# Kernel tuning notes

Hardware: AMD Instinct MI355X
Metric: run time of the kernel (lower is better)

## Reference

```python
import jax, jax.numpy as jnp
import numpy as np

T, I, H, O = 8192, 512, 1024, 2


def setup_inputs() -> dict:
    key = jax.random.key(0)
    ks = jax.random.split(key, 7)
    s_ih = 1.0 / np.sqrt(H)
    return {
        "input_seq": jax.random.normal(ks[0], (T, I), dtype=jnp.float32),
        "W_ih": jax.random.normal(ks[1], (4 * H, I), dtype=jnp.float32) * s_ih,
        "W_hh": jax.random.normal(ks[2], (4 * H, H), dtype=jnp.float32) * s_ih,
        "b_ih": jax.random.normal(ks[3], (4 * H,), dtype=jnp.float32) * s_ih,
        "b_hh": jax.random.normal(ks[4], (4 * H,), dtype=jnp.float32) * s_ih,
        "W_lin": jax.random.normal(ks[5], (O, H), dtype=jnp.float32) * s_ih,
        "b_lin": jax.random.normal(ks[6], (O,), dtype=jnp.float32) * s_ih,
    }


def reference(input_seq, W_ih, W_hh, b_ih, b_hh, W_lin, b_lin):
    h0 = jnp.zeros((H,), dtype=input_seq.dtype)
    c0 = jnp.zeros((H,), dtype=input_seq.dtype)
    # Precompute input projections for all timesteps: (T, 4H)
    x_gates = input_seq @ W_ih.T + b_ih + b_hh

    def step(carry, xg):
        h, c = carry
        gates = xg + h @ W_hh.T  # (4H,) in PyTorch order i, f, g, o
        i_g, f_g, g_g, o_g = jnp.split(gates, 4)
        i_g = jax.nn.sigmoid(i_g)
        f_g = jax.nn.sigmoid(f_g)
        g_g = jnp.tanh(g_g)
        o_g = jax.nn.sigmoid(o_g)
        c_new = f_g * c + i_g * g_g
        h_new = o_g * jnp.tanh(c_new)
        return (h_new, c_new), h_new

    _, hs = jax.lax.scan(step, (h0, c0), x_gates)  # hs: (T, H)
    logits = hs @ W_lin.T + b_lin  # (T, O)
    return jax.nn.softmax(logits, axis=-1)
```

## Files before the change

### kernel.cpp

```cpp
#include <hip/hip_runtime.h>
#include <stdint.h>

#define T_STEPS 8192
#define IN_DIM  512
#define HID     1024
#define G4      4096
#define NBLK    64
#define NW      16

typedef unsigned long long u64;

__global__ __launch_bounds__(256) void gemm_xgates(
    const float* __restrict__ A,
    const float* __restrict__ W,
    const float* __restrict__ bih,
    const float* __restrict__ bhh,
    float* __restrict__ xg)
{
    __shared__ float At[8][128];
    __shared__ float Bt[8][128];
    const int tid = threadIdx.x;
    const int r0 = blockIdx.x * 128;
    const int t0 = blockIdx.y * 128;
    const int tx = tid & 15, ty = tid >> 4;
    const int lrow = tid >> 1;
    const int kq   = (tid & 1) * 4;

    float acc[8][8];
#pragma unroll
    for (int i = 0; i < 8; ++i)
#pragma unroll
        for (int j = 0; j < 8; ++j) acc[i][j] = 0.f;

    for (int k0 = 0; k0 < IN_DIM; k0 += 8) {
        float4 av = *(const float4*)&A[(size_t)(t0 + lrow) * IN_DIM + k0 + kq];
        float4 bv = *(const float4*)&W[(size_t)(r0 + lrow) * IN_DIM + k0 + kq];
        __syncthreads();
        At[kq + 0][lrow] = av.x; At[kq + 1][lrow] = av.y;
        At[kq + 2][lrow] = av.z; At[kq + 3][lrow] = av.w;
        Bt[kq + 0][lrow] = bv.x; Bt[kq + 1][lrow] = bv.y;
        Bt[kq + 2][lrow] = bv.z; Bt[kq + 3][lrow] = bv.w;
        __syncthreads();
#pragma unroll
        for (int k = 0; k < 8; ++k) {
            float4 a0 = *(const float4*)&At[k][ty * 8];
            float4 a1 = *(const float4*)&At[k][ty * 8 + 4];
            float4 b0 = *(const float4*)&Bt[k][tx * 8];
            float4 b1 = *(const float4*)&Bt[k][tx * 8 + 4];
            float aa[8] = {a0.x, a0.y, a0.z, a0.w, a1.x, a1.y, a1.z, a1.w};
            float bb[8] = {b0.x, b0.y, b0.z, b0.w, b1.x, b1.y, b1.z, b1.w};
#pragma unroll
            for (int i = 0; i < 8; ++i)
#pragma unroll
                for (int j = 0; j < 8; ++j) acc[i][j] += aa[i] * bb[j];
        }
    }

    float bias[8];
#pragma unroll
    for (int j = 0; j < 8; ++j) {
        int r = r0 + tx * 8 + j;
        bias[j] = bih[r] + bhh[r];
    }
#pragma unroll
    for (int i = 0; i < 8; ++i) {
        int t = t0 + ty * 8 + i;
        float4 o0 = make_float4(acc[i][0] + bias[0], acc[i][1] + bias[1],
                                acc[i][2] + bias[2], acc[i][3] + bias[3]);
        float4 o1 = make_float4(acc[i][4] + bias[4], acc[i][5] + bias[5],
                                acc[i][6] + bias[6], acc[i][7] + bias[7]);
        *(float4*)&xg[(size_t)t * G4 + r0 + tx * 8]     = o0;
        *(float4*)&xg[(size_t)t * G4 + r0 + tx * 8 + 4] = o1;
    }
}

__device__ __forceinline__ float sigm_f(float x) {
    return __builtin_amdgcn_rcpf(1.f + __expf(-x));
}
__device__ __forceinline__ float tanh_f(float x) {
    x = fminf(fmaxf(x, -15.f), 15.f);
    float e = __expf(2.f * x);
    return (e - 1.f) * __builtin_amdgcn_rcpf(e + 1.f);
}

__device__ __forceinline__ float dpp_reduce_add(float x) {
    int v;
    v = __builtin_amdgcn_update_dpp(0, __float_as_int(x), 0x111, 0xf, 0xf, true);
    x += __int_as_float(v);
    v = __builtin_amdgcn_update_dpp(0, __float_as_int(x), 0x112, 0xf, 0xf, true);
    x += __int_as_float(v);
    v = __builtin_amdgcn_update_dpp(0, __float_as_int(x), 0x114, 0xf, 0xf, true);
    x += __int_as_float(v);
    v = __builtin_amdgcn_update_dpp(0, __float_as_int(x), 0x118, 0xf, 0xf, true);
    x += __int_as_float(v);
    v = __builtin_amdgcn_update_dpp(0, __float_as_int(x), 0x142, 0xa, 0xf, true);
    x += __int_as_float(v);
    v = __builtin_amdgcn_update_dpp(0, __float_as_int(x), 0x143, 0xc, 0xf, true);
    x += __int_as_float(v);
    return x;
}

__global__ __launch_bounds__(1024, 1) void lstm_rec(
    const float* __restrict__ Whh,
    const float* __restrict__ xg,
    float* __restrict__ hs,
    u64* __restrict__ hdata)
{
    __shared__ float2   hinp2[2][512];
    __shared__ float    hout_h[NW];
    __shared__ uint32_t hout_tag[NW];

    const int tid = threadIdx.x;
    const int b   = blockIdx.x;
    const int w   = tid >> 6;
    const int l   = tid & 63;
    const int j   = b * NW + w;
    const int ju  = __builtin_amdgcn_readfirstlane(j);

    if (tid < NW) hout_tag[tid] = 0;

    float2 wreg2[4][8];
#pragma unroll
    for (int s = 0; s < 4; ++s) {
        const float* row = &Whh[(size_t)(s * 1024 + j) * HID];
#pragma unroll
        for (int i = 0; i < 8; ++i) {
            wreg2[s][i].x = row[128 * i + l];
            wreg2[s][i].y = row[128 * i + 64 + l];
        }
    }
#pragma unroll
    for (int s = 0; s < 4; ++s)
#pragma unroll
        for (int i = 0; i < 8; ++i) {
            asm volatile("" : "+v"(wreg2[s][i].x));
            asm volatile("" : "+v"(wreg2[s][i].y));
        }

    float xv[4];
#pragma unroll
    for (int s = 0; s < 4; ++s)
        xv[s] = xg[(size_t)0 * G4 + s * 1024 + ju];

    float c = 0.f;

    for (int t = 0; t < T_STEPS; ++t) {
        const int buf = t & 1;
        if (t > 0 && w < 4) {
            const u64* base = hdata + (((size_t)(t - 1) & 1) << 10) + 256 * w;
            const u64 want = (u64)(uint32_t)t;
            u64 v0, v1, v2, v3;
            for (;;) {
                v0 = __hip_atomic_load(base + l,       __ATOMIC_RELAXED, __HIP_MEMORY_SCOPE_AGENT);
                v1 = __hip_atomic_load(base + 64 + l,  __ATOMIC_RELAXED, __HIP_MEMORY_SCOPE_AGENT);
                v2 = __hip_atomic_load(base + 128 + l, __ATOMIC_RELAXED, __HIP_MEMORY_SCOPE_AGENT);
                v3 = __hip_atomic_load(base + 192 + l, __ATOMIC_RELAXED, __HIP_MEMORY_SCOPE_AGENT);
                bool ok = ((v0 >> 32) == want) & ((v1 >> 32) == want) &
                          ((v2 >> 32) == want) & ((v3 >> 32) == want);
                if (__all(ok)) break;
            }
            hinp2[buf][128 * w + l] = make_float2(__uint_as_float((uint32_t)v0),
                                                  __uint_as_float((uint32_t)v1));
            hinp2[buf][128 * w + 64 + l] = make_float2(__uint_as_float((uint32_t)v2),
                                                       __uint_as_float((uint32_t)v3));
        }
        __syncthreads();

        float2 hval2[8];
        if (t > 0) {
#pragma unroll
            for (int i = 0; i < 8; ++i) hval2[i] = hinp2[buf][64 * i + l];
        } else {
#pragma unroll
            for (int i = 0; i < 8; ++i) hval2[i] = make_float2(0.f, 0.f);
        }

        float xn[4] = {0.f, 0.f, 0.f, 0.f};
        if (t < T_STEPS - 1) {
#pragma unroll
            for (int s = 0; s < 4; ++s)
                xn[s] = xg[(size_t)(t + 1) * G4 + s * 1024 + ju];
        }

        float gsum[4];
#pragma unroll
        for (int s = 0; s < 4; ++s) {
            float2 a2 = make_float2(0.f, 0.f);
#pragma unroll
            for (int i = 0; i < 8; ++i) {
                a2.x = fmaf(wreg2[s][i].x, hval2[i].x, a2.x);
                a2.y = fmaf(wreg2[s][i].y, hval2[i].y, a2.y);
            }
            gsum[s] = dpp_reduce_add(a2.x + a2.y);
        }

        float ig = sigm_f(xv[0] + gsum[0]);
        float fg = sigm_f(xv[1] + gsum[1]);
        float gv = tanh_f(xv[2] + gsum[2]);
        float og = sigm_f(xv[3] + gsum[3]);
        c = fg * c + ig * gv;
        float h = og * tanh_f(c);

        if (l == 63) {
            hout_h[w] = h;
            __hip_atomic_store(&hout_tag[w], (uint32_t)(t + 1),
                               __ATOMIC_RELEASE, __HIP_MEMORY_SCOPE_WORKGROUP);
        }

        if (w == 4) {
            const uint32_t want = (uint32_t)(t + 1);
            for (;;) {
                uint32_t tg = (l < NW)
                    ? __hip_atomic_load(&hout_tag[l], __ATOMIC_ACQUIRE,
                                        __HIP_MEMORY_SCOPE_WORKGROUP)
                    : want;
                if (__all(tg == want)) break;
            }
            if (l < NW) {
                float hv = hout_h[l];
                u64 pub = ((u64)want << 32) | (u64)__float_as_uint(hv);
                __hip_atomic_store(&hdata[((size_t)buf << 10) + b * NW + l], pub,
                                   __ATOMIC_RELAXED, __HIP_MEMORY_SCOPE_AGENT);
                hs[(size_t)(t + 1) * HID + b * NW + l] = hv;
            }
        }

#pragma unroll
        for (int s = 0; s < 4; ++s) xv[s] = xn[s];
    }
}

__global__ __launch_bounds__(256) void proj_softmax(
    const float* __restrict__ hs,
    const float* __restrict__ Wl,
    const float* __restrict__ bl,
    float* __restrict__ out)
{
    const int tid = threadIdx.x;
    const int w = tid >> 6, l = tid & 63;
    const int row = blockIdx.x * 4 + w;
    const float* h = &hs[(size_t)(row + 1) * HID];

    float a0 = 0.f, a1 = 0.f;
#pragma unroll
    for (int i = 0; i < 4; ++i) {
        float4 hv = *(const float4*)&h[256 * i + 4 * l];
        float4 w0 = *(const float4*)&Wl[256 * i + 4 * l];
        float4 w1 = *(const float4*)&Wl[HID + 256 * i + 4 * l];
        a0 = fmaf(hv.x, w0.x, a0); a0 = fmaf(hv.y, w0.y, a0);
        a0 = fmaf(hv.z, w0.z, a0); a0 = fmaf(hv.w, w0.w, a0);
        a1 = fmaf(hv.x, w1.x, a1); a1 = fmaf(hv.y, w1.y, a1);
        a1 = fmaf(hv.z, w1.z, a1); a1 = fmaf(hv.w, w1.w, a1);
    }
#pragma unroll
    for (int off = 1; off < 64; off <<= 1) {
        a0 += __shfl_xor(a0, off, 64);
        a1 += __shfl_xor(a1, off, 64);
    }
    if (l == 0) {
        float l0 = a0 + bl[0];
        float l1 = a1 + bl[1];
        float m  = fmaxf(l0, l1);
        float e0 = __expf(l0 - m), e1 = __expf(l1 - m);
        float inv = 1.f / (e0 + e1);
        float2 o = make_float2(e0 * inv, e1 * inv);
        *(float2*)&out[(size_t)row * 2] = o;
    }
}

extern "C" void kernel_launch(void* const* d_in, const int* in_sizes, int n_in,
                              void* d_out, int out_size, void* d_ws, size_t ws_size,
                              hipStream_t stream)
{
    const float* input = (const float*)d_in[0];
    const float* W_ih  = (const float*)d_in[1];
    const float* W_hh  = (const float*)d_in[2];
    const float* b_ih  = (const float*)d_in[3];
    const float* b_hh  = (const float*)d_in[4];
    const float* W_lin = (const float*)d_in[5];
    const float* b_lin = (const float*)d_in[6];
    float* out = (float*)d_out;

    char* ws = (char*)d_ws;
    float* hs     = (float*)ws;
    size_t hs_b   = (size_t)(T_STEPS + 1) * HID * sizeof(float);
    u64*   hdata  = (u64*)(ws + hs_b);
    size_t hd_b   = 2 * 1024 * sizeof(u64);
    float* xg     = (float*)(ws + hs_b + hd_b);


    dim3 g1(G4 / 128, T_STEPS / 128);
    gemm_xgates<<<g1, 256, 0, stream>>>(input, W_ih, b_ih, b_hh, xg);

    lstm_rec<<<NBLK, NW * 64, 0, stream>>>(W_hh, xg, hs, hdata);

    proj_softmax<<<T_STEPS / 4, 256, 0, stream>>>(hs, W_lin, b_lin, out);
}
```

Baseline: 18.15 ms.

## Split LSTM recurrence over K per wavefront and reduce partials in one wave

The recurrent kernel is restructured so each wavefront owns a 64-wide slice of the hidden vector for all 64 gate rows of the block, instead of each wave owning one hidden unit over the full K. Each wave polls only its own 64 h entries from global memory, computes partial dot products from register-held weights, and publishes them to shared memory with a per-wave flag. Wave 0 then sums the 16 partials per row, broadcasts the four gates within a quad via DPP, and publishes h. This removes the block-wide __syncthreads and the DPP tree reductions, and spreads the global polling across all waves. The cost is extra shared-memory traffic and a serial flag wait plus reduction on wave 0 in every step.

```diff
diff --git a/kernel.cpp b/kernel.cpp
--- a/kernel.cpp
+++ b/kernel.cpp
@@ -83,21 +83,10 @@
     return (e - 1.f) * __builtin_amdgcn_rcpf(e + 1.f);
 }
 
-__device__ __forceinline__ float dpp_reduce_add(float x) {
-    int v;
-    v = __builtin_amdgcn_update_dpp(0, __float_as_int(x), 0x111, 0xf, 0xf, true);
-    x += __int_as_float(v);
-    v = __builtin_amdgcn_update_dpp(0, __float_as_int(x), 0x112, 0xf, 0xf, true);
-    x += __int_as_float(v);
-    v = __builtin_amdgcn_update_dpp(0, __float_as_int(x), 0x114, 0xf, 0xf, true);
-    x += __int_as_float(v);
-    v = __builtin_amdgcn_update_dpp(0, __float_as_int(x), 0x118, 0xf, 0xf, true);
-    x += __int_as_float(v);
-    v = __builtin_amdgcn_update_dpp(0, __float_as_int(x), 0x142, 0xa, 0xf, true);
-    x += __int_as_float(v);
-    v = __builtin_amdgcn_update_dpp(0, __float_as_int(x), 0x143, 0xc, 0xf, true);
-    x += __int_as_float(v);
-    return x;
+template <int PAT>
+__device__ __forceinline__ float quad_bcast(float x) {
+    int v = __builtin_amdgcn_update_dpp(0, __float_as_int(x), PAT, 0xf, 0xf, true);
+    return __int_as_float(v);
 }
 
 __global__ __launch_bounds__(1024, 1) void lstm_rec(
@@ -106,127 +95,103 @@
     float* __restrict__ hs,
     u64* __restrict__ hdata)
 {
-    __shared__ float2   hinp2[2][512];
-    __shared__ float    hout_h[NW];
-    __shared__ uint32_t hout_tag[NW];
-
-    const int tid = threadIdx.x;
-    const int b   = blockIdx.x;
-    const int w   = tid >> 6;
-    const int l   = tid & 63;
-    const int j   = b * NW + w;
-    const int ju  = __builtin_amdgcn_readfirstlane(j);
-
-    if (tid < NW) hout_tag[tid] = 0;
-
-    float2 wreg2[4][8];
-#pragma unroll
-    for (int s = 0; s < 4; ++s) {
-        const float* row = &Whh[(size_t)(s * 1024 + j) * HID];
-#pragma unroll
-        for (int i = 0; i < 8; ++i) {
-            wreg2[s][i].x = row[128 * i + l];
-            wreg2[s][i].y = row[128 * i + 64 + l];
+    __shared__ float    chunk[NW][64];
+    __shared__ float    part[2][NW][64];
+    __shared__ uint32_t pflag[2][NW];
+
+    const int tid  = threadIdx.x;
+    const int b    = blockIdx.x;
+    const int w    = tid >> 6;
+    const int l    = tid & 63;
+    const int gate = l & 3;
+    const int h16  = l >> 2;
+    const int grow = gate * HID + b * NW + h16;
+
+    float4 wv[16];
+    {
+        const float* row = &Whh[(size_t)grow * HID + 64 * w];
+#pragma unroll
+        for (int k4 = 0; k4 < 16; ++k4) wv[k4] = *(const float4*)&row[4 * k4];
+    }
+#pragma unroll
+    for (int k4 = 0; k4 < 16; ++k4)
+        asm volatile("" : "+v"(wv[k4].x), "+v"(wv[k4].y),
+                         "+v"(wv[k4].z), "+v"(wv[k4].w));
+
+    if (tid < 2 * NW) ((uint32_t*)pflag)[tid] = 0;
+    __syncthreads();
+
+    const bool is_red = (w == 0);
+    float c  = 0.f;
+    float xv = 0.f, xn = 0.f;
+    if (is_red) xv = xg[grow];
+
+    for (int t = 0; t < T_STEPS; ++t) {
+        float a0 = 0.f, a1 = 0.f, a2 = 0.f, a3 = 0.f;
+        if (t > 0) {
+            const u64* ptr = hdata + (((size_t)(t - 1) & 1) << 10) + 64 * w + l;
+            const uint32_t want32 = (uint32_t)t;
+            u64 va = __hip_atomic_load(ptr, __ATOMIC_RELAXED, __HIP_MEMORY_SCOPE_AGENT);
+            u64 vb = __hip_atomic_load(ptr, __ATOMIC_RELAXED, __HIP_MEMORY_SCOPE_AGENT);
+            u64 v;
+            for (;;) {
+                if (__all((uint32_t)(va >> 32) == want32)) { v = va; break; }
+                va = __hip_atomic_load(ptr, __ATOMIC_RELAXED, __HIP_MEMORY_SCOPE_AGENT);
+                if (__all((uint32_t)(vb >> 32) == want32)) { v = vb; break; }
+                vb = __hip_atomic_load(ptr, __ATOMIC_RELAXED, __HIP_MEMORY_SCOPE_AGENT);
+            }
+            chunk[w][l] = __uint_as_float((uint32_t)v);
+#pragma unroll
+            for (int k4 = 0; k4 < 16; ++k4) {
+                float4 h4 = *(const float4*)&chunk[w][4 * k4];
+                a0 = fmaf(wv[k4].x, h4.x, a0);
+                a1 = fmaf(wv[k4].y, h4.y, a1);
+                a2 = fmaf(wv[k4].z, h4.z, a2);
+                a3 = fmaf(wv[k4].w, h4.w, a3);
+            }
         }
-    }
-#pragma unroll
-    for (int s = 0; s < 4; ++s)
-#pragma unroll
-        for (int i = 0; i < 8; ++i) {
-            asm volatile("" : "+v"(wreg2[s][i].x));
-            asm volatile("" : "+v"(wreg2[s][i].y));
+        const int p = t & 1;
+        part[p][w][l] = (a0 + a1) + (a2 + a3);
+        if (l == 0)
+            __hip_atomic_store(&pflag[p][w], (uint32_t)(t + 1),
+                               __ATOMIC_RELEASE, __HIP_MEMORY_SCOPE_WORKGROUP);
+
+        if (is_red) {
+            if (t + 1 < T_STEPS)
+                xn = xg[(size_t)(t + 1) * G4 + grow];
+            const uint32_t fw = (uint32_t)(t + 1);
+            for (;;) {
+                uint32_t f = (l < NW)
+                    ? __hip_atomic_load(&pflag[p][l], __ATOMIC_ACQUIRE,
+                                        __HIP_MEMORY_SCOPE_WORKGROUP)
+                    : fw;
+                if (__all(f == fw)) break;
+            }
+            float s0 = 0.f, s1 = 0.f, s2 = 0.f, s3 = 0.f;
+#pragma unroll
+            for (int ww = 0; ww < NW; ww += 4) {
+                s0 += part[p][ww + 0][l];
+                s1 += part[p][ww + 1][l];
+                s2 += part[p][ww + 2][l];
+                s3 += part[p][ww + 3][l];
+            }
+            float pre = ((s0 + s1) + (s2 + s3)) + xv;
+            float pi = quad_bcast<0x00>(pre);
+            float pf = quad_bcast<0x55>(pre);
+            float pg = quad_bcast<0xAA>(pre);
+            float po = quad_bcast<0xFF>(pre);
+            float ig = sigm_f(pi), fg = sigm_f(pf);
+            float gv = tanh_f(pg), og = sigm_f(po);
+            c = fg * c + ig * gv;
+            float h = og * tanh_f(c);
+            if (gate == 0) {
+                u64 pub = ((u64)fw << 32) | (u64)__float_as_uint(h);
+                __hip_atomic_store(&hdata[((size_t)p << 10) + b * NW + h16], pub,
+                                   __ATOMIC_RELAXED, __HIP_MEMORY_SCOPE_AGENT);
+                hs[(size_t)(t + 1) * HID + b * NW + h16] = h;
+            }
+            xv = xn;
         }
-
-    float xv[4];
-#pragma unroll
-    for (int s = 0; s < 4; ++s)
-        xv[s] = xg[(size_t)0 * G4 + s * 1024 + ju];
-
-    float c = 0.f;
-
-    for (int t = 0; t < T_STEPS; ++t) {
-        const int buf = t & 1;
-        if (t > 0 && w < 4) {
-            const u64* base = hdata + (((size_t)(t - 1) & 1) << 10) + 256 * w;
-            const u64 want = (u64)(uint32_t)t;
-            u64 v0, v1, v2, v3;
-            for (;;) {
-                v0 = __hip_atomic_load(base + l,       __ATOMIC_RELAXED, __HIP_MEMORY_SCOPE_AGENT);
-                v1 = __hip_atomic_load(base + 64 + l,  __ATOMIC_RELAXED, __HIP_MEMORY_SCOPE_AGENT);
-                v2 = __hip_atomic_load(base + 128 + l, __ATOMIC_RELAXED, __HIP_MEMORY_SCOPE_AGENT);
-                v3 = __hip_atomic_load(base + 192 + l, __ATOMIC_RELAXED, __HIP_MEMORY_SCOPE_AGENT);
-                bool ok = ((v0 >> 32) == want) & ((v1 >> 32) == want) &
-                          ((v2 >> 32) == want) & ((v3 >> 32) == want);
-                if (__all(ok)) break;
-            }
-            hinp2[buf][128 * w + l] = make_float2(__uint_as_float((uint32_t)v0),
-                                                  __uint_as_float((uint32_t)v1));
-            hinp2[buf][128 * w + 64 + l] = make_float2(__uint_as_float((uint32_t)v2),
-                                                       __uint_as_float((uint32_t)v3));
-        }
-        __syncthreads();
-
-        float2 hval2[8];
-        if (t > 0) {
-#pragma unroll
-            for (int i = 0; i < 8; ++i) hval2[i] = hinp2[buf][64 * i + l];
-        } else {
-#pragma unroll
-            for (int i = 0; i < 8; ++i) hval2[i] = make_float2(0.f, 0.f);
-        }
-
-        float xn[4] = {0.f, 0.f, 0.f, 0.f};
-        if (t < T_STEPS - 1) {
-#pragma unroll
-            for (int s = 0; s < 4; ++s)
-                xn[s] = xg[(size_t)(t + 1) * G4 + s * 1024 + ju];
-        }
-
-        float gsum[4];
-#pragma unroll
-        for (int s = 0; s < 4; ++s) {
-            float2 a2 = make_float2(0.f, 0.f);
-#pragma unroll
-            for (int i = 0; i < 8; ++i) {
-                a2.x = fmaf(wreg2[s][i].x, hval2[i].x, a2.x);
-                a2.y = fmaf(wreg2[s][i].y, hval2[i].y, a2.y);
-            }
-            gsum[s] = dpp_reduce_add(a2.x + a2.y);
-        }
-
-        float ig = sigm_f(xv[0] + gsum[0]);
-        float fg = sigm_f(xv[1] + gsum[1]);
-        float gv = tanh_f(xv[2] + gsum[2]);
-        float og = sigm_f(xv[3] + gsum[3]);
-        c = fg * c + ig * gv;
-        float h = og * tanh_f(c);
-
-        if (l == 63) {
-            hout_h[w] = h;
-            __hip_atomic_store(&hout_tag[w], (uint32_t)(t + 1),
-                               __ATOMIC_RELEASE, __HIP_MEMORY_SCOPE_WORKGROUP);
-        }
-
-        if (w == 4) {
-            const uint32_t want = (uint32_t)(t + 1);
-            for (;;) {
-                uint32_t tg = (l < NW)
-                    ? __hip_atomic_load(&hout_tag[l], __ATOMIC_ACQUIRE,
-                                        __HIP_MEMORY_SCOPE_WORKGROUP)
-                    : want;
-                if (__all(tg == want)) break;
-            }
-            if (l < NW) {
-                float hv = hout_h[l];
-                u64 pub = ((u64)want << 32) | (u64)__float_as_uint(hv);
-                __hip_atomic_store(&hdata[((size_t)buf << 10) + b * NW + l], pub,
-                                   __ATOMIC_RELAXED, __HIP_MEMORY_SCOPE_AGENT);
-                hs[(size_t)(t + 1) * HID + b * NW + l] = hv;
-            }
-        }
-
-#pragma unroll
-        for (int s = 0; s < 4; ++s) xv[s] = xn[s];
     }
 }
 
```

After: 16.46 ms. 1.1x faster.
